# Kernel tuning notes

Measured on AMD Instinct MI355X. Metric: run time of the kernel, lower is better.

The kernel has to match this reference:

```python
import jax, jax.numpy as jnp
import numpy as np

# Model dims
D = 2048        # hidden_size
H = 16          # num_heads
KVH = 8         # num_key_value_heads
DH = 128        # head_dim
NUM_SLOTS = 16  # state-cache slots
B = 4           # prefill segments (regularized ragged batch)
L = 2048        # tokens per segment
T = B * L
C = 64          # GLA chunk size (fused_chunk_gla)
NEG = -1e30


def setup_inputs() -> dict:
    key = jax.random.key(0)
    k0, k1, k2, k3 = jax.random.split(key, 4)
    hidden_states = jax.random.normal(k0, (T, D), jnp.float32)
    W_qkv = jax.random.normal(k1, (D, (H + 2 * KVH) * DH), jnp.float32) * 0.02
    b_qkv = jnp.zeros(((H + 2 * KVH) * DH,), jnp.float32)
    kv_cache = jax.random.normal(k2, (NUM_SLOTS, H, DH, DH), jnp.float32) * 0.1
    state_indices = jax.random.randint(k3, (B,), 0, NUM_SLOTS, jnp.int32)
    return {"hidden_states": hidden_states, "W_qkv": W_qkv, "b_qkv": b_qkv,
            "kv_cache": kv_cache, "state_indices": state_indices}


def _to_chunks(x):
    # [T, H, d] -> [n_chunks, B, C, H, d]
    return x.reshape(B, L // C, C, H, DH).transpose(1, 0, 2, 3, 4)


def _gla_chunk_body(mask):
    def body(S, inp):
        # S: [B,H,dk,dv]; qc/kc/vc/gc: [B,C,H,d]
        qc, kc, vc, gc = inp
        Bc = jnp.cumsum(gc, axis=1)                       # inclusive log-decay within chunk
        # inter-chunk: initial state decayed by exp(Bc)
        o_inter = jnp.einsum('bchk,bhkv->bchv', qc * jnp.exp(Bc), S)
        # intra-chunk causal scores: A_ij = sum_d q_i,d * exp(B_i - B_j)_d * k_j,d, j<=i
        diff = Bc[:, :, None] - Bc[:, None, :]            # [B,Ci,Cj,H,dk], <=0 on lower tri
        diff = jnp.where(mask[None, :, :, None, None], diff, NEG)
        A = jnp.einsum('bihk,bijhk,bjhk->bijh', qc, jnp.exp(diff), kc)
        o = o_inter + jnp.einsum('bijh,bjhv->bihv', A, vc)
        # state update: S' = diag(exp(B_last)) S + sum_j (k_j exp(B_last - B_j)) v_j^T
        b_last = Bc[:, -1]                                # [B,H,dk]
        kg = kc * jnp.exp(b_last[:, None] - Bc)
        S_new = S * jnp.exp(b_last)[..., None] + jnp.einsum('bchk,bchv->bhkv', kg, vc)
        return S_new, o
    return jax.checkpoint(body)


def _forward(hidden_states, W_qkv, b_qkv, kv_cache, state_indices):
    qkv = hidden_states @ W_qkv + b_qkv
    q = qkv[:, :H * DH].reshape(T, H, DH)
    k = qkv[:, H * DH:(H + KVH) * DH].reshape(T, KVH, DH)
    v = qkv[:, (H + KVH) * DH:].reshape(T, KVH, DH)
    n_rep = H // KVH
    k = jnp.repeat(k, n_rep, axis=1)                      # repeat_kv (3D branch)
    v = jnp.repeat(v, n_rep, axis=1)
    q = jax.nn.relu(q) * DH ** -0.5                       # q_feature_map + fused_chunk_gla scale
    k = jnp.minimum(jax.nn.sigmoid(k), 0.95)              # sigmoid + clamp(max=clamp_max)
    g = jnp.log1p(-k)                                     # (1 - k).log()

    S0 = kv_cache[state_indices]                          # [B,H,dk,dv] per-slot initial states
    mask = jnp.tril(jnp.ones((C, C), bool))
    _, o = jax.lax.scan(_gla_chunk_body(mask), S0,
                        (_to_chunks(q), _to_chunks(k), _to_chunks(v), _to_chunks(g)))
    # [n_chunks,B,C,H,dv] -> per-segment concat [T, H*dv]
    return o.transpose(1, 0, 2, 3, 4).reshape(T, H * DH)


def reference(hidden_states, W_qkv, b_qkv, kv_cache, state_indices):
    return _forward(hidden_states, W_qkv, b_qkv, kv_cache, state_indices)
```

## Files before the change

kernel.cpp:

```cpp
#include <hip/hip_runtime.h>
#include <hip/hip_bf16.h>
#include <math.h>

#define RSQRT_DH 0.08838834764831845f

typedef __attribute__((ext_vector_type(8))) short short8;
typedef __attribute__((ext_vector_type(4))) float floatx4;

static __device__ __forceinline__ float bf2f(unsigned short u) {
  return __uint_as_float(((unsigned int)u) << 16);
}
static __device__ __forceinline__ unsigned short f2bf(float f) {
  unsigned int x = __float_as_uint(f);
  return (unsigned short)((x + 0x7fffu + ((x >> 16) & 1u)) >> 16);
}
static __device__ __forceinline__ ushort4 f4bf(float a, float b, float c, float d) {
  ushort4 r; r.x = f2bf(a); r.y = f2bf(b); r.z = f2bf(c); r.w = f2bf(d); return r;
}
static __device__ __forceinline__ short8 ld8u(const unsigned short* p) {
  short4 a = *(const short4*)p;
  short4 b = *(const short4*)(p + 4);
  short8 r;
  r[0] = a.x; r[1] = a.y; r[2] = a.z; r[3] = a.w;
  r[4] = b.x; r[5] = b.y; r[6] = b.z; r[7] = b.w;
  return r;
}

__launch_bounds__(256)
__global__ void k_cvt(const float* __restrict__ in, unsigned short* __restrict__ out, int n4) {
  int i = blockIdx.x * 256 + threadIdx.x;
  if (i >= n4) return;
  float4 v = ((const float4*)in)[i];
  ((ushort4*)out)[i] = f4bf(v.x, v.y, v.z, v.w);
}

__launch_bounds__(256)
__global__ void k_cvt_wt(const float* __restrict__ W, unsigned short* __restrict__ Wt) {
  __shared__ float tile[32][33];
  int t = threadIdx.x;
  int c = t & 31, r = t >> 5;
  int bx = blockIdx.x, by = blockIdx.y;
#pragma unroll
  for (int j = 0; j < 4; ++j)
    tile[r + j * 8][c] = W[(size_t)(by * 32 + r + j * 8) * 4096 + bx * 32 + c];
  __syncthreads();
#pragma unroll
  for (int j = 0; j < 4; ++j)
    Wt[(size_t)(bx * 32 + r + j * 8) * 2048 + by * 32 + c] = f2bf(tile[c][r + j * 8]);
}

__launch_bounds__(256)
__global__ void k_gemm(const unsigned short* __restrict__ A,
                       const unsigned short* __restrict__ Bt,
                       const float* __restrict__ bias,
                       unsigned short* __restrict__ qb,
                       unsigned short* __restrict__ kb,
                       unsigned short* __restrict__ vb,
                       float* __restrict__ gf) {
  __shared__ unsigned short lds_a[128 * 64];
  __shared__ unsigned short lds_b[128 * 64];
  const int t = threadIdx.x;
  const int m0 = blockIdx.y * 128;
  const int n0 = blockIdx.x * 128;
  const int w = t >> 6, l = t & 63;
  const int wr = w >> 1, wc = w & 1;

  const int srow = l >> 3;
  const int scol = (l & 7) * 8;
  const unsigned short* agp = A + (size_t)(m0 + w * 8 + srow) * 2048 + scol;
  const unsigned short* bgp = Bt + (size_t)(n0 + w * 8 + srow) * 2048 + scol;

  floatx4 acc[4][4] = {};

  for (int kt = 0; kt < 2048; kt += 64) {
    __syncthreads();
#pragma unroll
    for (int it = 0; it < 4; ++it) {
      __builtin_amdgcn_global_load_lds(
          (const __attribute__((address_space(1))) void*)(agp + kt + (size_t)it * 32 * 2048),
          (__attribute__((address_space(3))) void*)(lds_a + (it * 32 + w * 8) * 64),
          16, 0, 0);
      __builtin_amdgcn_global_load_lds(
          (const __attribute__((address_space(1))) void*)(bgp + kt + (size_t)it * 32 * 2048),
          (__attribute__((address_space(3))) void*)(lds_b + (it * 32 + w * 8) * 64),
          16, 0, 0);
    }
    __syncthreads();
#pragma unroll
    for (int ks = 0; ks < 2; ++ks) {
      short8 af[4], bf[4];
      const int krow = ks * 32 + (l >> 4) * 8;
#pragma unroll
      for (int ti = 0; ti < 4; ++ti)
        af[ti] = *(const short8*)(lds_a + (wr * 64 + ti * 16 + (l & 15)) * 64 + krow);
#pragma unroll
      for (int tj = 0; tj < 4; ++tj)
        bf[tj] = *(const short8*)(lds_b + (wc * 64 + tj * 16 + (l & 15)) * 64 + krow);
#pragma unroll
      for (int ti = 0; ti < 4; ++ti)
#pragma unroll
        for (int tj = 0; tj < 4; ++tj)
          acc[ti][tj] = __builtin_amdgcn_mfma_f32_16x16x32_bf16(af[ti], bf[tj], acc[ti][tj], 0, 0, 0);
    }
  }
#pragma unroll
  for (int ti = 0; ti < 4; ++ti) {
#pragma unroll
    for (int tj = 0; tj < 4; ++tj) {
      const int n = n0 + wc * 64 + tj * 16 + (l & 15);
      const float bn = bias[n];
#pragma unroll
      for (int r = 0; r < 4; ++r) {
        const int m = m0 + wr * 64 + ti * 16 + ((l >> 4) * 4) + r;
        float val = acc[ti][tj][r] + bn;
        if (n < 2048) {
          qb[(size_t)m * 2048 + n] = f2bf(fmaxf(val, 0.f) * RSQRT_DH);
        } else if (n < 3072) {
          float s = 1.f / (1.f + __expf(-val));
          s = fminf(s, 0.95f);
          size_t idx = (size_t)m * 1024 + (n - 2048);
          kb[idx] = f2bf(s);
          gf[idx] = log1pf(-s);
        } else {
          vb[(size_t)m * 1024 + (n - 3072)] = f2bf(val);
        }
      }
    }
  }
}

__launch_bounds__(256)
__global__ void k_phaseA(const unsigned short* __restrict__ kb,
                         const unsigned short* __restrict__ vb,
                         const float* __restrict__ gf,
                         float* __restrict__ blast,
                         unsigned short* __restrict__ Pb) {
  __shared__ float sBc[64 * 128];
  __shared__ float sKg[64 * 128];
  const int t = threadIdx.x;
  const int chunk = blockIdx.x, chain = blockIdx.y;
  const int b = chain >> 4, h = chain & 15, kvh = h >> 1;
  const int t0 = b * 2048 + chunk * 64;

#pragma unroll
  for (int rep = 0; rep < 8; ++rep) {
    int e = rep * 256 + t;
    int i = e >> 5, d4 = e & 31;
    *(float4*)(sBc + i * 128 + d4 * 4) =
        *(const float4*)(gf + (size_t)(t0 + i) * 1024 + kvh * 128 + d4 * 4);
  }
  __syncthreads();
  if (t < 128) {
    float run = sBc[t];
    for (int i = 1; i < 64; ++i) { run += sBc[i * 128 + t]; sBc[i * 128 + t] = run; }
    blast[((size_t)chain * 32 + chunk) * 128 + t] = run;
  }
  __syncthreads();
#pragma unroll
  for (int rep = 0; rep < 32; ++rep) {
    int e = rep * 256 + t;
    int i = e >> 7, d = e & 127;
    float kk = bf2f(kb[(size_t)(t0 + i) * 1024 + kvh * 128 + d]);
    sKg[e] = kk * __expf(sBc[63 * 128 + d] - sBc[e]);
  }
  __syncthreads();
  const int kq = t >> 3, vq = t & 7;
  const int kd0 = kq * 4, vd0 = vq * 16;
  float acc[4][16] = {};
  const unsigned short* vrow = vb + (size_t)t0 * 1024 + kvh * 128 + vd0;
  for (int i = 0; i < 64; ++i) {
    float4 kg4 = *(const float4*)(sKg + i * 128 + kd0);
    float ka[4] = {kg4.x, kg4.y, kg4.z, kg4.w};
    ushort4 v0 = *(const ushort4*)(vrow + (size_t)i * 1024);
    ushort4 v1 = *(const ushort4*)(vrow + (size_t)i * 1024 + 4);
    ushort4 v2 = *(const ushort4*)(vrow + (size_t)i * 1024 + 8);
    ushort4 v3 = *(const ushort4*)(vrow + (size_t)i * 1024 + 12);
    float vf[16] = {bf2f(v0.x), bf2f(v0.y), bf2f(v0.z), bf2f(v0.w),
                    bf2f(v1.x), bf2f(v1.y), bf2f(v1.z), bf2f(v1.w),
                    bf2f(v2.x), bf2f(v2.y), bf2f(v2.z), bf2f(v2.w),
                    bf2f(v3.x), bf2f(v3.y), bf2f(v3.z), bf2f(v3.w)};
#pragma unroll
    for (int r = 0; r < 4; ++r)
#pragma unroll
      for (int j = 0; j < 16; ++j) acc[r][j] += ka[r] * vf[j];
  }
  size_t pbase = ((size_t)chain * 32 + chunk) * 16384;
#pragma unroll
  for (int r = 0; r < 4; ++r)
#pragma unroll
    for (int j4 = 0; j4 < 4; ++j4)
      *(ushort4*)(Pb + pbase + (size_t)(kd0 + r) * 128 + vd0 + j4 * 4) =
          f4bf(acc[r][j4 * 4], acc[r][j4 * 4 + 1], acc[r][j4 * 4 + 2], acc[r][j4 * 4 + 3]);
}

__launch_bounds__(256)
__global__ void k_scan(const float* __restrict__ kv_cache,
                       const int* __restrict__ sidx,
                       const float* __restrict__ blast,
                       const unsigned short* __restrict__ Pb,
                       unsigned short* __restrict__ Sb) {
  const int t = threadIdx.x;
  const int part = blockIdx.x;
  const int chain = blockIdx.y;
  const int b = chain >> 4, h = chain & 15;
  const int e0 = part * 1024 + t * 4;
  const int kd = e0 >> 7;
  const int slot = sidx[b];
  float4 s = *(const float4*)(kv_cache + ((size_t)slot * 16 + h) * 16384 + e0);
#pragma unroll 1
  for (int c = 0; c < 32; ++c) {
    *(ushort4*)(Sb + ((size_t)c * 64 + chain) * 16384 + e0) = f4bf(s.x, s.y, s.z, s.w);
    float eb = __expf(blast[((size_t)chain * 32 + c) * 128 + kd]);
    ushort4 p = *(const ushort4*)(Pb + ((size_t)chain * 32 + c) * 16384 + e0);
    s.x = s.x * eb + bf2f(p.x);
    s.y = s.y * eb + bf2f(p.y);
    s.z = s.z * eb + bf2f(p.z);
    s.w = s.w * eb + bf2f(p.w);
  }
}

__launch_bounds__(256)
__global__ void k_output(const unsigned short* __restrict__ qb,
                         const unsigned short* __restrict__ kb,
                         const unsigned short* __restrict__ vb,
                         const float* __restrict__ gf,
                         const unsigned short* __restrict__ Sb,
                         float* __restrict__ out) {
  __shared__ float sBc[64 * 128];
  __shared__ unsigned short sR3[11136];
  unsigned short* sA   = sR3;
  unsigned short* sKE  = sR3 + 4608;
  unsigned short* sQE2 = sR3 + 4608 + 4352;
  unsigned short* sQE0 = sR3;
  unsigned short* sSt  = sR3 + 4608;
  unsigned short* sVt  = sR3 + 4608;

  const int t = threadIdx.x;
  const int w = t >> 6, l = t & 63;
  const int lr = l & 15, quad = l >> 4;
  const int chunk = blockIdx.x, chain = blockIdx.y;
  const int b = chain >> 4, h = chain & 15, kvh = h >> 1;
  const int t0 = b * 2048 + chunk * 64;
  const size_t sbase = ((size_t)chunk * 64 + chain) * 16384;

#pragma unroll
  for (int rep = 0; rep < 8; ++rep) {
    int e = rep * 256 + t, i = e >> 5, d4 = e & 31;
    *(float4*)(sBc + i * 128 + d4 * 4) =
        *(const float4*)(gf + (size_t)(t0 + i) * 1024 + kvh * 128 + d4 * 4);
  }
  __syncthreads();
  if (t < 128) {
    float run = sBc[t];
#pragma unroll
    for (int i = 1; i < 64; ++i) { run += sBc[i * 128 + t]; sBc[i * 128 + t] = run; }
  }

  floatx4 o[8];
#pragma unroll
  for (int i = 0; i < 8; ++i) o[i] = 0.f;

#pragma unroll
  for (int kh = 0; kh < 2; ++kh) {
    __syncthreads();
#pragma unroll
    for (int rep = 0; rep < 2; ++rep) {
      int idx = rep * 256 + t;
      int i = idx >> 3, g = idx & 7;
      int k0 = kh * 64 + g * 8;
      short8 q8 = *(const short8*)(qb + (size_t)(t0 + i) * 2048 + h * 128 + k0);
      short8 r;
#pragma unroll
      for (int u = 0; u < 8; ++u)
        r[u] = (short)f2bf(bf2f((unsigned short)q8[u]) * __expf(sBc[i * 128 + k0 + u]));
      *(short8*)(sQE0 + i * 72 + g * 8) = r;
    }
#pragma unroll
    for (int vh = 0; vh < 2; ++vh) {
      __syncthreads();
#pragma unroll
      for (int rep = 0; rep < 2; ++rep) {
        int idx = rep * 256 + t;
        int kl = idx >> 3, g = idx & 7;
        short8 s8 = *(const short8*)(Sb + sbase + (size_t)(kh * 64 + kl) * 128 + vh * 64 + g * 8);
#pragma unroll
        for (int u = 0; u < 8; ++u) sSt[(g * 8 + u) * 76 + kl] = (unsigned short)s8[u];
      }
      __syncthreads();
      short8 af0 = *(const short8*)(sQE0 + (w * 16 + lr) * 72 + quad * 8);
      short8 af1 = *(const short8*)(sQE0 + (w * 16 + lr) * 72 + 32 + quad * 8);
#pragma unroll
      for (int tv = 0; tv < 4; ++tv) {
        const unsigned short* bp = sSt + (tv * 16 + lr) * 76 + quad * 8;
        short8 bf0 = ld8u(bp);
        short8 bf1 = ld8u(bp + 32);
        o[vh * 4 + tv] = __builtin_amdgcn_mfma_f32_16x16x32_bf16(af0, bf0, o[vh * 4 + tv], 0, 0, 0);
        o[vh * 4 + tv] = __builtin_amdgcn_mfma_f32_16x16x32_bf16(af1, bf1, o[vh * 4 + tv], 0, 0, 0);
      }
    }
  }

  __syncthreads();
  for (int idx = t; idx < 576; idx += 256)
    *(short8*)(sA + idx * 8) = (short8)0;
#pragma unroll
  for (int I = 0; I < 4; ++I) {
    const float* Rrow = (I > 0) ? (sBc + (I * 16 - 1) * 128) : nullptr;
    for (int base = 0; base < (I + 1) * 16; base += 32) {
      int nrows = min(32, (I + 1) * 16 - base);
      __syncthreads();
      int ngroups = nrows * 16;
      for (int idx = t; idx < ngroups; idx += 256) {
        int jl = idx >> 4, g = idx & 15;
        int j = base + jl, k0 = g * 8;
        short8 k8 = *(const short8*)(kb + (size_t)(t0 + j) * 1024 + kvh * 128 + k0);
        short8 r;
#pragma unroll
        for (int u = 0; u < 8; ++u) {
          int k = k0 + u;
          float Rk = Rrow ? Rrow[k] : 0.f;
          r[u] = (short)f2bf(bf2f((unsigned short)k8[u]) * __expf(Rk - sBc[j * 128 + k]));
        }
        *(short8*)(sKE + jl * 136 + k0) = r;
      }
      if (base == 0) {
        {
          int idx = t;
          int il = idx >> 4, g = idx & 15;
          int i = I * 16 + il, k0 = g * 8;
          short8 q8 = *(const short8*)(qb + (size_t)(t0 + i) * 2048 + h * 128 + k0);
          short8 r;
#pragma unroll
          for (int u = 0; u < 8; ++u) {
            int k = k0 + u;
            float Rk = Rrow ? Rrow[k] : 0.f;
            r[u] = (short)f2bf(bf2f((unsigned short)q8[u]) * __expf(sBc[i * 128 + k] - Rk));
          }
          *(short8*)(sQE2 + il * 136 + k0) = r;
        }
      }
      __syncthreads();
      const int J = w;
      if (J * 16 >= base && J * 16 < base + nrows) {
        floatx4 a4 = {};
#pragma unroll
        for (int ks = 0; ks < 4; ++ks) {
          short8 afr = *(const short8*)(sQE2 + lr * 136 + ks * 32 + quad * 8);
          short8 bfr = *(const short8*)(sKE + (J * 16 - base + lr) * 136 + ks * 32 + quad * 8);
          a4 = __builtin_amdgcn_mfma_f32_16x16x32_bf16(afr, bfr, a4, 0, 0, 0);
        }
#pragma unroll
        for (int r = 0; r < 4; ++r) {
          int il = quad * 4 + r;
          float v = ((J < I) || (lr <= il)) ? a4[r] : 0.f;
          sA[(I * 16 + il) * 72 + J * 16 + lr] = f2bf(v);
        }
      }
    }
  }

  __syncthreads();
  short8 aA0 = *(const short8*)(sA + (w * 16 + lr) * 72 + quad * 8);
  short8 aA1 = *(const short8*)(sA + (w * 16 + lr) * 72 + 32 + quad * 8);
#pragma unroll
  for (int vh = 0; vh < 2; ++vh) {
    if (vh) __syncthreads();
#pragma unroll
    for (int rep = 0; rep < 2; ++rep) {
      int idx = rep * 256 + t;
      int j = idx >> 3, g = idx & 7;
      short8 v8 = *(const short8*)(vb + (size_t)(t0 + j) * 1024 + kvh * 128 + vh * 64 + g * 8);
#pragma unroll
      for (int u = 0; u < 8; ++u) sVt[(g * 8 + u) * 76 + j] = (unsigned short)v8[u];
    }
    __syncthreads();
#pragma unroll
    for (int tv = 0; tv < 4; ++tv) {
      const unsigned short* bp = sVt + (tv * 16 + lr) * 76 + quad * 8;
      short8 b0 = ld8u(bp);
      short8 b1 = ld8u(bp + 32);
      o[vh * 4 + tv] = __builtin_amdgcn_mfma_f32_16x16x32_bf16(aA0, b0, o[vh * 4 + tv], 0, 0, 0);
      o[vh * 4 + tv] = __builtin_amdgcn_mfma_f32_16x16x32_bf16(aA1, b1, o[vh * 4 + tv], 0, 0, 0);
    }
  }

#pragma unroll
  for (int tv8 = 0; tv8 < 8; ++tv8) {
    int col = (tv8 >> 2) * 64 + (tv8 & 3) * 16 + lr;
#pragma unroll
    for (int r = 0; r < 4; ++r) {
      int i = w * 16 + quad * 4 + r;
      out[(size_t)(t0 + i) * 2048 + h * 128 + col] = o[tv8][r];
    }
  }
}

extern "C" void kernel_launch(void* const* d_in, const int* in_sizes, int n_in,
                              void* d_out, int out_size, void* d_ws, size_t ws_size,
                              hipStream_t stream) {
  (void)in_sizes; (void)n_in; (void)out_size; (void)ws_size;
  const float* hs   = (const float*)d_in[0];
  const float* W    = (const float*)d_in[1];
  const float* bias = (const float*)d_in[2];
  const float* kvc  = (const float*)d_in[3];
  const int*   sidx = (const int*)d_in[4];

  char* ws = (char*)d_ws;
  unsigned short* Sb  = (unsigned short*)(ws + 0);
  unsigned short* hsb = (unsigned short*)(ws + 0);
  unsigned short* wtb = (unsigned short*)(ws + 33554432);
  unsigned short* qb  = (unsigned short*)(ws + 67108864);
  unsigned short* kb  = (unsigned short*)(ws + 100663296);
  unsigned short* vb  = (unsigned short*)(ws + 117440512);
  float*          gf  = (float*)(ws + 134217728);
  float*          bl  = (float*)(ws + 167772160);
  unsigned short* Pb  = (unsigned short*)d_out;
  float* out = (float*)d_out;

  k_cvt<<<dim3(16384), dim3(256), 0, stream>>>(hs, hsb, 16777216 / 4);
  k_cvt_wt<<<dim3(128, 64), dim3(256), 0, stream>>>(W, wtb);
  k_gemm<<<dim3(32, 64), dim3(256), 0, stream>>>(hsb, wtb, bias, qb, kb, vb, gf);
  k_phaseA<<<dim3(32, 64), dim3(256), 0, stream>>>(kb, vb, gf, bl, Pb);
  k_scan<<<dim3(16, 64), dim3(256), 0, stream>>>(kvc, sidx, bl, Pb, Sb);
  k_output<<<dim3(32, 64), dim3(256), 0, stream>>>(qb, kb, vb, gf, Sb, out);
}
```

Measured before the change: 662.0 us.

## Rewrite QKV GEMM with 256x256 tiles, 4-stage LDS pipeline and swizzles

Replaces the single-buffered 128x128 bf16 GEMM with a 256x256-tile, 512-thread kernel. It uses a 4-deep LDS ring of 32-wide K tiles filled by async global_load_lds, with explicit vmcnt waits so loads overlap MFMA work. It also adds an XOR swizzle on LDS columns to cut bank conflicts, block-id swizzling for L2 reuse, and s_setprio around MFMA bursts. The cost is higher register pressure from 32 accumulators per lane, 128KB of LDS, and fragile hand-tuned wait counts.

```diff
diff --git a/kernel.cpp b/kernel.cpp
--- a/kernel.cpp
+++ b/kernel.cpp
@@ -6,6 +6,8 @@
 
 typedef __attribute__((ext_vector_type(8))) short short8;
 typedef __attribute__((ext_vector_type(4))) float floatx4;
+
+#define BAR() do { asm volatile("" ::: "memory"); __builtin_amdgcn_s_barrier(); asm volatile("" ::: "memory"); } while (0)
 
 static __device__ __forceinline__ float bf2f(unsigned short u) {
   return __uint_as_float(((unsigned int)u) << 16);
@@ -49,7 +51,7 @@
     Wt[(size_t)(bx * 32 + r + j * 8) * 2048 + by * 32 + c] = f2bf(tile[c][r + j * 8]);
 }
 
-__launch_bounds__(256)
+__launch_bounds__(512, 2)
 __global__ void k_gemm(const unsigned short* __restrict__ A,
                        const unsigned short* __restrict__ Bt,
                        const float* __restrict__ bias,
@@ -57,72 +59,112 @@
                        unsigned short* __restrict__ kb,
                        unsigned short* __restrict__ vb,
                        float* __restrict__ gf) {
-  __shared__ unsigned short lds_a[128 * 64];
-  __shared__ unsigned short lds_b[128 * 64];
-  const int t = threadIdx.x;
-  const int m0 = blockIdx.y * 128;
-  const int n0 = blockIdx.x * 128;
-  const int w = t >> 6, l = t & 63;
-  const int wr = w >> 1, wc = w & 1;
-
-  const int srow = l >> 3;
-  const int scol = (l & 7) * 8;
-  const unsigned short* agp = A + (size_t)(m0 + w * 8 + srow) * 2048 + scol;
-  const unsigned short* bgp = Bt + (size_t)(n0 + w * 8 + srow) * 2048 + scol;
-
-  floatx4 acc[4][4] = {};
-
-  for (int kt = 0; kt < 2048; kt += 64) {
-    __syncthreads();
-#pragma unroll
-    for (int it = 0; it < 4; ++it) {
-      __builtin_amdgcn_global_load_lds(
-          (const __attribute__((address_space(1))) void*)(agp + kt + (size_t)it * 32 * 2048),
-          (__attribute__((address_space(3))) void*)(lds_a + (it * 32 + w * 8) * 64),
-          16, 0, 0);
-      __builtin_amdgcn_global_load_lds(
-          (const __attribute__((address_space(1))) void*)(bgp + kt + (size_t)it * 32 * 2048),
-          (__attribute__((address_space(3))) void*)(lds_b + (it * 32 + w * 8) * 64),
-          16, 0, 0);
-    }
-    __syncthreads();
-#pragma unroll
-    for (int ks = 0; ks < 2; ++ks) {
-      short8 af[4], bf[4];
-      const int krow = ks * 32 + (l >> 4) * 8;
-#pragma unroll
-      for (int ti = 0; ti < 4; ++ti)
-        af[ti] = *(const short8*)(lds_a + (wr * 64 + ti * 16 + (l & 15)) * 64 + krow);
-#pragma unroll
-      for (int tj = 0; tj < 4; ++tj)
-        bf[tj] = *(const short8*)(lds_b + (wc * 64 + tj * 16 + (l & 15)) * 64 + krow);
-#pragma unroll
-      for (int ti = 0; ti < 4; ++ti)
-#pragma unroll
-        for (int tj = 0; tj < 4; ++tj)
-          acc[ti][tj] = __builtin_amdgcn_mfma_f32_16x16x32_bf16(af[ti], bf[tj], acc[ti][tj], 0, 0, 0);
-    }
-  }
-#pragma unroll
-  for (int ti = 0; ti < 4; ++ti) {
-#pragma unroll
-    for (int tj = 0; tj < 4; ++tj) {
-      const int n = n0 + wc * 64 + tj * 16 + (l & 15);
-      const float bn = bias[n];
+  __shared__ unsigned short lds[65536];
+
+  const int tid = threadIdx.x;
+  const int w = tid >> 6, l = tid & 63;
+  const int wm = w >> 2, wn = w & 3;
+  const int lr = l & 15, quad = l >> 4;
+
+  const int id = blockIdx.x;
+  const int swz = (id & 7) * 64 + (id >> 3);
+  const int bm = swz >> 4, bn = swz & 15;
+  const int m0 = bm * 256, n0 = bn * 256;
+
+  const int srow = tid >> 2;
+  const int scol = (((tid & 3) ^ ((tid >> 3) & 3)) << 3);
+  const unsigned short* agp = A + (size_t)(m0 + srow) * 2048 + scol;
+  const unsigned short* bgp = Bt + (size_t)(n0 + srow) * 2048 + scol;
+  unsigned short* ldsA_dst = lds + w * 512;
+  unsigned short* ldsB_dst = lds + 8192 + w * 512;
+
+  auto stageA = [&](int d, int u, int ktile) {
+    __builtin_amdgcn_global_load_lds(
+        (const __attribute__((address_space(1))) void*)(agp + (size_t)u * 262144 + (size_t)ktile * 32),
+        (__attribute__((address_space(3))) void*)(ldsA_dst + d * 16384 + u * 4096),
+        16, 0, 0);
+  };
+  auto stageB = [&](int d, int u, int ktile) {
+    __builtin_amdgcn_global_load_lds(
+        (const __attribute__((address_space(1))) void*)(bgp + (size_t)u * 262144 + (size_t)ktile * 32),
+        (__attribute__((address_space(3))) void*)(ldsB_dst + d * 16384 + u * 4096),
+        16, 0, 0);
+  };
+
+  const int kcol = ((quad ^ ((lr >> 1) & 3)) << 3);
+  const int arow_base = (wm * 128 + lr) * 32 + kcol;
+  const int brow_base = (wn * 64 + lr) * 32 + kcol;
+
+  floatx4 acc[8][4] = {};
+
+#pragma unroll
+  for (int pt = 0; pt < 3; ++pt) {
+    stageA(pt, 0, pt); stageA(pt, 1, pt);
+    stageB(pt, 0, pt); stageB(pt, 1, pt);
+  }
+
+  for (int t = 0; t < 64; ++t) {
+    const int d = t & 3;
+    const unsigned short* Ab = lds + d * 16384;
+    const unsigned short* Bb = Ab + 8192;
+    const int t3 = t + 3;
+    const int d3 = t3 & 3;
+
+    if (t < 62)       asm volatile("s_waitcnt vmcnt(8)" ::: "memory");
+    else if (t == 62) asm volatile("s_waitcnt vmcnt(4)" ::: "memory");
+    else              asm volatile("s_waitcnt vmcnt(0)" ::: "memory");
+    BAR();
+
+    short8 af[4], bfr[4];
+#pragma unroll
+    for (int i = 0; i < 4; ++i) af[i] = *(const short8*)(Ab + arow_base + i * 512);
+#pragma unroll
+    for (int i = 0; i < 4; ++i) bfr[i] = *(const short8*)(Bb + brow_base + i * 512);
+    if (t3 < 64) { stageA(d3, 0, t3); stageA(d3, 1, t3); }
+    __builtin_amdgcn_s_setprio(1);
+#pragma unroll
+    for (int mi = 0; mi < 4; ++mi)
+#pragma unroll
+      for (int ni = 0; ni < 4; ++ni)
+        acc[mi][ni] = __builtin_amdgcn_mfma_f32_16x16x32_bf16(af[mi], bfr[ni], acc[mi][ni], 0, 0, 0);
+    __builtin_amdgcn_s_setprio(0);
+
+    BAR();
+
+#pragma unroll
+    for (int i = 0; i < 4; ++i) af[i] = *(const short8*)(Ab + arow_base + 2048 + i * 512);
+    if (t3 < 64) { stageB(d3, 0, t3); stageB(d3, 1, t3); }
+    __builtin_amdgcn_s_setprio(1);
+#pragma unroll
+    for (int mi = 0; mi < 4; ++mi)
+#pragma unroll
+      for (int ni = 0; ni < 4; ++ni)
+        acc[4 + mi][ni] = __builtin_amdgcn_mfma_f32_16x16x32_bf16(af[mi], bfr[ni], acc[4 + mi][ni], 0, 0, 0);
+    __builtin_amdgcn_s_setprio(0);
+  }
+
+  const int lm0 = m0 + wm * 128 + quad * 4;
+  const int ln0 = n0 + wn * 64 + lr;
+#pragma unroll
+  for (int ni = 0; ni < 4; ++ni) {
+    const int col = ln0 + ni * 16;
+    const float bnv = bias[col];
+#pragma unroll
+    for (int mi = 0; mi < 8; ++mi) {
 #pragma unroll
       for (int r = 0; r < 4; ++r) {
-        const int m = m0 + wr * 64 + ti * 16 + ((l >> 4) * 4) + r;
-        float val = acc[ti][tj][r] + bn;
-        if (n < 2048) {
-          qb[(size_t)m * 2048 + n] = f2bf(fmaxf(val, 0.f) * RSQRT_DH);
-        } else if (n < 3072) {
+        const int row = lm0 + mi * 16 + r;
+        float val = acc[mi][ni][r] + bnv;
+        if (col < 2048) {
+          qb[(size_t)row * 2048 + col] = f2bf(fmaxf(val, 0.f) * RSQRT_DH);
+        } else if (col < 3072) {
           float s = 1.f / (1.f + __expf(-val));
           s = fminf(s, 0.95f);
-          size_t idx = (size_t)m * 1024 + (n - 2048);
+          size_t idx = (size_t)row * 1024 + (col - 2048);
           kb[idx] = f2bf(s);
           gf[idx] = log1pf(-s);
         } else {
-          vb[(size_t)m * 1024 + (n - 3072)] = f2bf(val);
+          vb[(size_t)row * 1024 + (col - 3072)] = f2bf(val);
         }
       }
     }
@@ -419,7 +461,7 @@
 
   k_cvt<<<dim3(16384), dim3(256), 0, stream>>>(hs, hsb, 16777216 / 4);
   k_cvt_wt<<<dim3(128, 64), dim3(256), 0, stream>>>(W, wtb);
-  k_gemm<<<dim3(32, 64), dim3(256), 0, stream>>>(hsb, wtb, bias, qb, kb, vb, gf);
+  k_gemm<<<dim3(512), dim3(512), 0, stream>>>(hsb, wtb, bias, qb, kb, vb, gf);
   k_phaseA<<<dim3(32, 64), dim3(256), 0, stream>>>(kb, vb, gf, bl, Pb);
   k_scan<<<dim3(16, 64), dim3(256), 0, stream>>>(kvc, sidx, bl, Pb, Sb);
   k_output<<<dim3(32, 64), dim3(256), 0, stream>>>(qb, kb, vb, gf, Sb, out);
```

Result: slower. 698.1 us (+5.5%).
